# Performance work log

Measured on AMD Instinct MI355X. Metric: run time of the kernel, lower is better.

The kernel has to match this reference:

```python
import jax, jax.numpy as jnp
import numpy as np

N_NODES = 50000
N_EDGES = 800000
D_IN, D_HID, D_OUT = 64, 128, 64


def _sage_conv(x, src, dst, W_l, b_l, W_r):
    # PyG SAGEConv (aggr='mean'): out = lin_l(mean_j x_j) + lin_r(x_i)
    msg = x[src]                                    # [E, d] gather
    summed = jax.ops.segment_sum(msg, dst, num_segments=N_NODES)
    cnt = jax.ops.segment_sum(jnp.ones((msg.shape[0], 1), x.dtype), dst,
                              num_segments=N_NODES)
    mean = summed / jnp.maximum(cnt, 1.0)           # [N, d]
    return mean @ W_l + b_l + x @ W_r


def setup_inputs() -> dict:
    key = jax.random.key(0)
    ks = jax.random.split(key, 8)
    x = jax.random.normal(ks[0], (N_NODES, D_IN), dtype=jnp.float32)
    edge_index = jax.random.randint(ks[1], (2, N_EDGES), 0, N_NODES, dtype=jnp.int64)
    s1 = 1.0 / np.sqrt(D_IN)
    s2 = 1.0 / np.sqrt(D_HID)
    W_l1 = jax.random.uniform(ks[2], (D_IN, D_HID), jnp.float32, -s1, s1)
    b_l1 = jnp.zeros((D_HID,), jnp.float32)
    W_r1 = jax.random.uniform(ks[3], (D_IN, D_HID), jnp.float32, -s1, s1)
    W_l2 = jax.random.uniform(ks[4], (D_HID, D_OUT), jnp.float32, -s2, s2)
    b_l2 = jnp.zeros((D_OUT,), jnp.float32)
    W_r2 = jax.random.uniform(ks[5], (D_HID, D_OUT), jnp.float32, -s2, s2)
    return {"x": x, "edge_index": edge_index,
            "W_l1": W_l1, "b_l1": b_l1, "W_r1": W_r1,
            "W_l2": W_l2, "b_l2": b_l2, "W_r2": W_r2}


def reference(x, edge_index, W_l1, b_l1, W_r1, W_l2, b_l2, W_r2):
    src, dst = edge_index[0], edge_index[1]
    h = _sage_conv(x, src, dst, W_l1, b_l1, W_r1)
    h = jax.nn.relu(h)
    # dropout is identity in eval mode (F.dropout(training=self.training))
    out = _sage_conv(h, src, dst, W_l2, b_l2, W_r2)
    return out
```

## Files before the change

### kernel.cpp

```cpp
#include <hip/hip_runtime.h>

namespace {

constexpr int NNODES = 50000;
constexpr int NEDGES = 800000;
constexpr int NBUCK  = (NNODES + 127) / 128;
constexpr int BCAP   = 3072;
constexpr int SB     = 64;
constexpr int CHUNK  = NEDGES / SB;


static __device__ __forceinline__ unsigned short f2bf(float f) {
  unsigned u = __float_as_uint(f);
  u += 0x7FFFu + ((u >> 16) & 1u);
  return (unsigned short)(u >> 16);
}

static __device__ __forceinline__ void pk_fma_lo(float2& d, const float2 a, const float2 b) {
  asm("v_pk_fma_f32 %0, %1, %2, %0 op_sel:[0,0,0] op_sel_hi:[0,1,1]"
      : "+v"(d) : "v"(a), "v"(b));
}
static __device__ __forceinline__ void pk_fma_hi(float2& d, const float2 a, const float2 b) {
  asm("v_pk_fma_f32 %0, %1, %2, %0 op_sel:[1,0,0] op_sel_hi:[1,1,1]"
      : "+v"(d) : "v"(a), "v"(b));
}

static __device__ __forceinline__ void grid_sync(int* bar, int target) {
  __syncthreads();
  if (threadIdx.x == 0) {
    __threadfence();
    atomicAdd(bar, 1);
    while (atomicAdd(bar, 0) < target) {
      __builtin_amdgcn_s_sleep(2);
    }
    __threadfence();
  }
  __syncthreads();
}

static __device__ __forceinline__ int detect_is64_block(const void* raw, int* s_tmp) {
  if (threadIdx.x == 0) *s_tmp = 0;
  __syncthreads();
  const unsigned int* w = (const unsigned int*)raw;
  const int nz = (w[1 + 2 * (int)(threadIdx.x & 511)] != 0u) ? 1 : 0;
  if (nz) atomicOr(s_tmp, 1);
  __syncthreads();
  return (*s_tmp == 0) ? 1 : 0;
}

__global__ __launch_bounds__(512) void prep_mega(const void* __restrict__ raw,
                                                 const float* __restrict__ xin,
                                                 unsigned short* __restrict__ xb,
                                                 int* __restrict__ blkhist,
                                                 int* __restrict__ offs,
                                                 int* __restrict__ bcount,
                                                 unsigned int* __restrict__ ecol,
                                                 int* __restrict__ rowse,
                                                 int* __restrict__ bar) {
  __shared__ int hist[NBUCK];
  __shared__ int loff[NBUCK];
  __shared__ int lcur[NBUCK];
  __shared__ int dcnt[128];
  __shared__ int noff[128];
  __shared__ int ncur[128];
  __shared__ int s_tmp;

  const int b = blockIdx.x;
  const int tid = (int)threadIdx.x;
  const int is64 = detect_is64_block(raw, &s_tmp);

  for (int t = b * 512 + tid; t < NNODES * 64 / 4; t += SB * 512) {
    const float4 v = ((const float4*)xin)[t];
    ushort4 o;
    o.x = f2bf(v.x); o.y = f2bf(v.y); o.z = f2bf(v.z); o.w = f2bf(v.w);
    ((ushort4*)xb)[t] = o;
  }
  for (int i = tid; i < NBUCK; i += 512) hist[i] = 0;
  __syncthreads();
  {
    const int beg = b * CHUNK, end = beg + CHUNK;
    for (int e = beg + tid; e < end; e += 512) {
      const int d = is64 ? (int)((const long long*)raw)[NEDGES + e]
                         : ((const int*)raw)[NEDGES + e];
      atomicAdd(&hist[d >> 7], 1);
    }
  }
  __syncthreads();
  for (int i = tid; i < NBUCK; i += 512) blkhist[i * SB + b] = hist[i];

  grid_sync(bar, SB * 1);

  {
    const int lane = tid & 63;
    const int bk = b * 8 + (tid >> 6);
    if (bk < NBUCK) {
      const int c = blkhist[bk * SB + lane];
      int s = c;
#pragma unroll
      for (int off = 1; off < 64; off <<= 1) {
        const int u = __shfl_up(s, off, 64);
        if (lane >= off) s += u;
      }
      offs[bk * SB + lane] = bk * BCAP + (s - c);
      if (lane == 63) bcount[bk] = s;
    }
  }

  grid_sync(bar, SB * 2);

  for (int i = tid; i < NBUCK; i += 512) {
    loff[i] = offs[i * SB + b];
    lcur[i] = 0;
  }
  __syncthreads();
  {
    const int beg = b * CHUNK, end = beg + CHUNK;
    for (int e = beg + tid; e < end; e += 512) {
      int s, d;
      if (is64) {
        const long long* p = (const long long*)raw;
        s = (int)p[e];
        d = (int)p[NEDGES + e];
      } else {
        const int* p = (const int*)raw;
        s = p[e];
        d = p[NEDGES + e];
      }
      const int bk = d >> 7;
      const unsigned int val = ((unsigned int)d << 16) | (unsigned int)s;
      const int lr = atomicAdd(&lcur[bk], 1);
      ecol[loff[bk] + lr] = val;
    }
  }

  grid_sync(bar, SB * 3);

  for (int bk = b; bk < NBUCK; bk += SB) {
    const int base = bk * 128;
    const int nloc = min(128, NNODES - base);
    const int cnt = bcount[bk];
    unsigned int* eb = ecol + (size_t)bk * BCAP;
    if (tid < 128) dcnt[tid] = 0;
    __syncthreads();
    unsigned int vals[6];
    int m = 0;
#pragma unroll
    for (int k = 0; k < 6; ++k) {
      const int e = tid + k * 512;
      if (e < cnt) {
        vals[k] = eb[e];
        atomicAdd(&dcnt[(vals[k] >> 16) & 127u], 1);
        m = k + 1;
      }
    }
    __syncthreads();
    if (tid < 128) noff[tid] = dcnt[tid];
    __syncthreads();
#pragma unroll
    for (int off = 1; off < 128; off <<= 1) {
      int add = 0;
      if (tid < 128 && tid >= off) add = noff[tid - off];
      __syncthreads();
      if (tid < 128) noff[tid] += add;
      __syncthreads();
    }
    if (tid < 128) {
      const int excl = noff[tid] - dcnt[tid];
      noff[tid] = excl;
      ncur[tid] = 0;
      if (tid < nloc)
        rowse[base + tid] = ((bk * BCAP + excl) << 9) | dcnt[tid];
    }
    __syncthreads();
#pragma unroll
    for (int k = 0; k < 6; ++k) {
      if (k < m) {
        const int loc = (int)((vals[k] >> 16) & 127u);
        eb[noff[loc] + atomicAdd(&ncur[loc], 1)] = vals[k] & 0xFFFFu;
      }
    }
    __syncthreads();
  }
}

template <bool FINAL>
__global__ __launch_bounds__(256) void seg_mean_bf(const unsigned int* __restrict__ xb2,
                                                   const int* __restrict__ rowse,
                                                   const unsigned int* __restrict__ col,
                                                   const float* __restrict__ radd,
                                                   float* __restrict__ outbuf) {
  const int lane = (int)(threadIdx.x & 63);
  const int half = lane >> 5;
  const int c = lane & 31;
  const int wid = (blockIdx.x * blockDim.x + threadIdx.x) >> 6;
  const int nw = (gridDim.x * blockDim.x) >> 6;
  for (int v = wid; v < NNODES; v += nw) {
    const int se = rowse[v];
    const int b = se >> 9;
    const int e = b + (se & 511);
    float accx = 0.0f, accy = 0.0f;
    int i = b;
    for (; i + 8 <= e; i += 8) {
      const int s0 = (int)col[i + 0 + half];
      const int s1 = (int)col[i + 2 + half];
      const int s2 = (int)col[i + 4 + half];
      const int s3 = (int)col[i + 6 + half];
      const unsigned int w0 = xb2[(size_t)s0 * 32 + c];
      const unsigned int w1 = xb2[(size_t)s1 * 32 + c];
      const unsigned int w2 = xb2[(size_t)s2 * 32 + c];
      const unsigned int w3 = xb2[(size_t)s3 * 32 + c];
      accx += __uint_as_float(w0 << 16) + __uint_as_float(w1 << 16)
            + __uint_as_float(w2 << 16) + __uint_as_float(w3 << 16);
      accy += __uint_as_float(w0 & 0xFFFF0000u) + __uint_as_float(w1 & 0xFFFF0000u)
            + __uint_as_float(w2 & 0xFFFF0000u) + __uint_as_float(w3 & 0xFFFF0000u);
    }
    for (; i + 2 <= e; i += 2) {
      const unsigned int w0 = xb2[(size_t)col[i + half] * 32 + c];
      accx += __uint_as_float(w0 << 16);
      accy += __uint_as_float(w0 & 0xFFFF0000u);
    }
    if (i < e && half == 0) {
      const unsigned int w0 = xb2[(size_t)col[i] * 32 + c];
      accx += __uint_as_float(w0 << 16);
      accy += __uint_as_float(w0 & 0xFFFF0000u);
    }
    accx += __shfl_xor(accx, 32, 64);
    accy += __shfl_xor(accy, 32, 64);
    if (half == 0) {
      const float inv = 1.0f / fmaxf((float)(se & 511), 1.0f);
      float2 res = make_float2(accx * inv, accy * inv);
      const size_t gi = (size_t)v * 32 + c;
      if (FINAL) {
        const float2 ra = ((const float2*)radd)[gi];
        res.x += ra.x; res.y += ra.y;
      }
      ((float2*)outbuf)[gi] = res;
    }
  }
}

template <int MODE>
__global__ __launch_bounds__(256, 3) void gemm128(const float* __restrict__ A0,
                                                  const float* __restrict__ A1,
                                                  const float* __restrict__ W0,
                                                  const float* __restrict__ W1,
                                                  const float* __restrict__ bias,
                                                  float* __restrict__ O0,
                                                  float* __restrict__ O1,
                                                  unsigned short* __restrict__ PB) {
  constexpr int SAS = 36;
  __shared__ float sA[64][SAS];
  __shared__ float sW[32][128];
  const int row0 = blockIdx.x * 64;
  const int tid = threadIdx.x;
  const int r0 = (tid >> 4) * 4;
  const int j0 = (tid & 15) * 4;

  float2 accA2[4][2];
  float2 accB2[4][2];
#pragma unroll
  for (int r = 0; r < 4; ++r)
#pragma unroll
    for (int p = 0; p < 2; ++p) {
      accA2[r][p] = make_float2(0.f, 0.f);
      accB2[r][p] = make_float2(0.f, 0.f);
    }

#pragma unroll 1
  for (int ck = 0; ck < 4; ++ck) {
#pragma unroll
    for (int v = 0; v < 2; ++v) {
      const int vid = v * 256 + tid;
      const int rr = vid >> 3;
      const int kq = (vid & 7) * 4;
      const int grow = row0 + rr;
      float4 val = make_float4(0.f, 0.f, 0.f, 0.f);
      if (grow < NNODES) {
        if (MODE == 0) {
          const float* src = (ck < 2) ? A0 : A1;
          const int kk = (ck & 1) * 32 + kq;
          val = *(const float4*)&src[(size_t)grow * 64 + kk];
        } else {
          val = *(const float4*)&A0[(size_t)grow * 128 + ck * 32 + kq];
        }
      }
      *(float4*)&sA[rr][kq] = val;
    }
#pragma unroll
    for (int v = 0; v < 4; ++v) {
      const int vid = v * 256 + tid;
      const int kk = vid >> 5;
      const int jq = (vid & 31) * 4;
      float4 w;
      if (MODE == 0) {
        const float* src = (ck < 2) ? W0 : W1;
        const int krel = (ck & 1) * 32 + kk;
        w = *(const float4*)&src[(size_t)krel * 128 + jq];
      } else {
        const int kg = ck * 32 + kk;
        const float* src = (jq < 64) ? W0 : W1;
        const int jrel = (jq < 64) ? jq : jq - 64;
        w = *(const float4*)&src[(size_t)kg * 64 + jrel];
      }
      *(float4*)&sW[kk][jq] = w;
    }
    __syncthreads();
#pragma unroll
    for (int k4 = 0; k4 < 8; ++k4) {
      float4 a[4];
#pragma unroll
      for (int r = 0; r < 4; ++r) a[r] = *(const float4*)&sA[r0 + r][k4 * 4];
#pragma unroll
      for (int kp = 0; kp < 2; ++kp) {
        const int k_even = k4 * 4 + kp * 2;
        const float4 wlo0 = *(const float4*)&sW[k_even][j0];
        const float4 whi0 = *(const float4*)&sW[k_even][64 + j0];
        const float4 wlo1 = *(const float4*)&sW[k_even + 1][j0];
        const float4 whi1 = *(const float4*)&sW[k_even + 1][64 + j0];
#pragma unroll
        for (int r = 0; r < 4; ++r) {
          const float2 ap = (kp == 0) ? make_float2(a[r].x, a[r].y)
                                      : make_float2(a[r].z, a[r].w);
          pk_fma_lo(accA2[r][0], ap, make_float2(wlo0.x, wlo0.y));
          pk_fma_lo(accA2[r][1], ap, make_float2(wlo0.z, wlo0.w));
          pk_fma_lo(accB2[r][0], ap, make_float2(whi0.x, whi0.y));
          pk_fma_lo(accB2[r][1], ap, make_float2(whi0.z, whi0.w));
          pk_fma_hi(accA2[r][0], ap, make_float2(wlo1.x, wlo1.y));
          pk_fma_hi(accA2[r][1], ap, make_float2(wlo1.z, wlo1.w));
          pk_fma_hi(accB2[r][0], ap, make_float2(whi1.x, whi1.y));
          pk_fma_hi(accB2[r][1], ap, make_float2(whi1.z, whi1.w));
        }
      }
    }
    __syncthreads();
  }

  float4 blo = make_float4(0.f, 0.f, 0.f, 0.f);
  float4 bhi;
  if (MODE == 0) {
    blo = *(const float4*)&bias[j0];
    bhi = *(const float4*)&bias[64 + j0];
  } else {
    bhi = *(const float4*)&bias[j0];
  }
#pragma unroll
  for (int r = 0; r < 4; ++r) {
    const int grow = row0 + r0 + r;
    if (grow >= NNODES) continue;
    float4 lo = make_float4(accA2[r][0].x + blo.x, accA2[r][0].y + blo.y,
                            accA2[r][1].x + blo.z, accA2[r][1].y + blo.w);
    float4 hi = make_float4(accB2[r][0].x + bhi.x, accB2[r][0].y + bhi.y,
                            accB2[r][1].x + bhi.z, accB2[r][1].y + bhi.w);
    if (MODE == 0) {
      lo.x = fmaxf(lo.x, 0.f); lo.y = fmaxf(lo.y, 0.f);
      lo.z = fmaxf(lo.z, 0.f); lo.w = fmaxf(lo.w, 0.f);
      hi.x = fmaxf(hi.x, 0.f); hi.y = fmaxf(hi.y, 0.f);
      hi.z = fmaxf(hi.z, 0.f); hi.w = fmaxf(hi.w, 0.f);
      *(float4*)&O0[(size_t)grow * 128 + j0] = lo;
      *(float4*)&O0[(size_t)grow * 128 + 64 + j0] = hi;
    } else {
      ushort4 ob;
      ob.x = f2bf(lo.x); ob.y = f2bf(lo.y); ob.z = f2bf(lo.z); ob.w = f2bf(lo.w);
      *(ushort4*)&PB[(size_t)grow * 64 + j0] = ob;
      *(float4*)&O1[(size_t)grow * 64 + j0] = hi;
    }
  }
}

}

extern "C" void kernel_launch(void* const* d_in, const int* in_sizes, int n_in,
                              void* d_out, int out_size, void* d_ws, size_t ws_size,
                              hipStream_t stream) {
  const float* x   = (const float*)d_in[0];
  const void*  ei  = d_in[1];
  const float* Wl1 = (const float*)d_in[2];
  const float* bl1 = (const float*)d_in[3];
  const float* Wr1 = (const float*)d_in[4];
  const float* Wl2 = (const float*)d_in[5];
  const float* bl2 = (const float*)d_in[6];
  const float* Wr2 = (const float*)d_in[7];
  float* out = (float*)d_out;

  char* ws = (char*)d_ws;
  int*            bar     = (int*)(ws + 0);
  int*            blkhist = (int*)(ws + 256);
  int*            offs    = (int*)(ws + 100608);
  int*            bcount  = (int*)(ws + 200960);
  int*            rowse   = (int*)(ws + 203008);
  unsigned int*   ecol    = (unsigned int*)(ws + 403200);
  unsigned short* xb      = (unsigned short*)(ws + 5207808);
  unsigned short* pb      = (unsigned short*)(ws + 11607808);
  float*          mean1   = (float*)(ws + 18007808);
  float*          h       = (float*)(ws + 30807808);
  float*          r       = mean1;

  hipMemsetAsync(bar, 0, 256, stream);

  prep_mega<<<SB, 512, 0, stream>>>(ei, x, xb, blkhist, offs, bcount, ecol, rowse, bar);

  constexpr int GEMM_BLOCKS = (NNODES + 63) / 64;

  seg_mean_bf<false><<<12500, 256, 0, stream>>>((const unsigned int*)xb, rowse, ecol,
                                                nullptr, mean1);
  gemm128<0><<<GEMM_BLOCKS, 256, 0, stream>>>(mean1, x, Wl1, Wr1, bl1, h, nullptr, nullptr);

  gemm128<1><<<GEMM_BLOCKS, 256, 0, stream>>>(h, nullptr, Wl2, Wr2, bl2, nullptr, r, pb);
  seg_mean_bf<true><<<12500, 256, 0, stream>>>((const unsigned int*)pb, rowse, ecol,
                                               r, out);
}
```

Baseline: 192.2 us.

## Split prep into separate kernels and fuse both layer GEMMs through shared memory

```diff
diff --git a/kernel.cpp b/kernel.cpp
--- a/kernel.cpp
+++ b/kernel.cpp
@@ -8,6 +8,7 @@
 constexpr int BCAP   = 3072;
 constexpr int SB     = 64;
 constexpr int CHUNK  = NEDGES / SB;
+constexpr int CONVB  = 1024;
 
 
 static __device__ __forceinline__ unsigned short f2bf(float f) {
@@ -25,19 +26,6 @@
       : "+v"(d) : "v"(a), "v"(b));
 }
 
-static __device__ __forceinline__ void grid_sync(int* bar, int target) {
-  __syncthreads();
-  if (threadIdx.x == 0) {
-    __threadfence();
-    atomicAdd(bar, 1);
-    while (atomicAdd(bar, 0) < target) {
-      __builtin_amdgcn_s_sleep(2);
-    }
-    __threadfence();
-  }
-  __syncthreads();
-}
-
 static __device__ __forceinline__ int detect_is64_block(const void* raw, int* s_tmp) {
   if (threadIdx.x == 0) *s_tmp = 0;
   __syncthreads();
@@ -48,138 +36,133 @@
   return (*s_tmp == 0) ? 1 : 0;
 }
 
-__global__ __launch_bounds__(512) void prep_mega(const void* __restrict__ raw,
-                                                 const float* __restrict__ xin,
-                                                 unsigned short* __restrict__ xb,
-                                                 int* __restrict__ blkhist,
-                                                 int* __restrict__ offs,
-                                                 int* __restrict__ bcount,
-                                                 unsigned int* __restrict__ ecol,
-                                                 int* __restrict__ rowse,
-                                                 int* __restrict__ bar) {
+__global__ __launch_bounds__(512) void histconv(const void* __restrict__ raw,
+                                                const float* __restrict__ xin,
+                                                unsigned short* __restrict__ xb,
+                                                int* __restrict__ blkhist) {
+  const int tid = (int)threadIdx.x;
+  if (blockIdx.x >= SB) {
+    const int b = blockIdx.x - SB;
+    for (int t = b * 512 + tid; t < NNODES * 64 / 4; t += CONVB * 512) {
+      const float4 v = ((const float4*)xin)[t];
+      ushort4 o;
+      o.x = f2bf(v.x); o.y = f2bf(v.y); o.z = f2bf(v.z); o.w = f2bf(v.w);
+      ((ushort4*)xb)[t] = o;
+    }
+    return;
+  }
   __shared__ int hist[NBUCK];
+  __shared__ int s_tmp;
+  const int is64 = detect_is64_block(raw, &s_tmp);
+  for (int i = tid; i < NBUCK; i += 512) hist[i] = 0;
+  __syncthreads();
+  const int b = blockIdx.x;
+  const int beg = b * CHUNK, end = beg + CHUNK;
+  for (int e = beg + tid; e < end; e += 512) {
+    const int d = is64 ? (int)((const long long*)raw)[NEDGES + e]
+                       : ((const int*)raw)[NEDGES + e];
+    atomicAdd(&hist[d >> 7], 1);
+  }
+  __syncthreads();
+  for (int i = tid; i < NBUCK; i += 512) blkhist[i * SB + b] = hist[i];
+}
+
+__global__ __launch_bounds__(512) void scatter_pass(const void* __restrict__ raw,
+                                                    const int* __restrict__ blkhist,
+                                                    unsigned int* __restrict__ ecol) {
   __shared__ int loff[NBUCK];
   __shared__ int lcur[NBUCK];
+  __shared__ int s_tmp;
+  const int is64 = detect_is64_block(raw, &s_tmp);
+  const int b = blockIdx.x;
+  const int tid = (int)threadIdx.x;
+  for (int bk = tid; bk < NBUCK; bk += 512) {
+    int s = 0;
+    for (int bb = 0; bb < b; ++bb) s += blkhist[bk * SB + bb];
+    loff[bk] = bk * BCAP + s;
+    lcur[bk] = 0;
+  }
+  __syncthreads();
+  const int beg = b * CHUNK, end = beg + CHUNK;
+  for (int e = beg + tid; e < end; e += 512) {
+    int s, d;
+    if (is64) {
+      const long long* p = (const long long*)raw;
+      s = (int)p[e];
+      d = (int)p[NEDGES + e];
+    } else {
+      const int* p = (const int*)raw;
+      s = p[e];
+      d = p[NEDGES + e];
+    }
+    const int bk = d >> 7;
+    const unsigned int val = ((unsigned int)d << 16) | (unsigned int)s;
+    const int lr = atomicAdd(&lcur[bk], 1);
+    ecol[loff[bk] + lr] = val;
+  }
+}
+
+__global__ __launch_bounds__(256) void csr_emit(const int* __restrict__ blkhist,
+                                                unsigned int* __restrict__ ecol,
+                                                int* __restrict__ rowse) {
+  const int bk = blockIdx.x;
+  const int base = bk * 128;
+  const int nloc = min(128, NNODES - base);
+  const int tid = (int)threadIdx.x;
+  unsigned int* eb = ecol + (size_t)bk * BCAP;
+
   __shared__ int dcnt[128];
   __shared__ int noff[128];
   __shared__ int ncur[128];
-  __shared__ int s_tmp;
-
-  const int b = blockIdx.x;
-  const int tid = (int)threadIdx.x;
-  const int is64 = detect_is64_block(raw, &s_tmp);
-
-  for (int t = b * 512 + tid; t < NNODES * 64 / 4; t += SB * 512) {
-    const float4 v = ((const float4*)xin)[t];
-    ushort4 o;
-    o.x = f2bf(v.x); o.y = f2bf(v.y); o.z = f2bf(v.z); o.w = f2bf(v.w);
-    ((ushort4*)xb)[t] = o;
-  }
-  for (int i = tid; i < NBUCK; i += 512) hist[i] = 0;
-  __syncthreads();
-  {
-    const int beg = b * CHUNK, end = beg + CHUNK;
-    for (int e = beg + tid; e < end; e += 512) {
-      const int d = is64 ? (int)((const long long*)raw)[NEDGES + e]
-                         : ((const int*)raw)[NEDGES + e];
-      atomicAdd(&hist[d >> 7], 1);
-    }
-  }
-  __syncthreads();
-  for (int i = tid; i < NBUCK; i += 512) blkhist[i * SB + b] = hist[i];
-
-  grid_sync(bar, SB * 1);
-
-  {
-    const int lane = tid & 63;
-    const int bk = b * 8 + (tid >> 6);
-    if (bk < NBUCK) {
-      const int c = blkhist[bk * SB + lane];
-      int s = c;
-#pragma unroll
-      for (int off = 1; off < 64; off <<= 1) {
-        const int u = __shfl_up(s, off, 64);
-        if (lane >= off) s += u;
-      }
-      offs[bk * SB + lane] = bk * BCAP + (s - c);
-      if (lane == 63) bcount[bk] = s;
-    }
-  }
-
-  grid_sync(bar, SB * 2);
-
-  for (int i = tid; i < NBUCK; i += 512) {
-    loff[i] = offs[i * SB + b];
-    lcur[i] = 0;
-  }
-  __syncthreads();
-  {
-    const int beg = b * CHUNK, end = beg + CHUNK;
-    for (int e = beg + tid; e < end; e += 512) {
-      int s, d;
-      if (is64) {
-        const long long* p = (const long long*)raw;
-        s = (int)p[e];
-        d = (int)p[NEDGES + e];
-      } else {
-        const int* p = (const int*)raw;
-        s = p[e];
-        d = p[NEDGES + e];
-      }
-      const int bk = d >> 7;
-      const unsigned int val = ((unsigned int)d << 16) | (unsigned int)s;
-      const int lr = atomicAdd(&lcur[bk], 1);
-      ecol[loff[bk] + lr] = val;
-    }
-  }
-
-  grid_sync(bar, SB * 3);
-
-  for (int bk = b; bk < NBUCK; bk += SB) {
-    const int base = bk * 128;
-    const int nloc = min(128, NNODES - base);
-    const int cnt = bcount[bk];
-    unsigned int* eb = ecol + (size_t)bk * BCAP;
-    if (tid < 128) dcnt[tid] = 0;
-    __syncthreads();
-    unsigned int vals[6];
-    int m = 0;
-#pragma unroll
-    for (int k = 0; k < 6; ++k) {
-      const int e = tid + k * 512;
-      if (e < cnt) {
-        vals[k] = eb[e];
-        atomicAdd(&dcnt[(vals[k] >> 16) & 127u], 1);
-        m = k + 1;
-      }
-    }
-    __syncthreads();
-    if (tid < 128) noff[tid] = dcnt[tid];
-    __syncthreads();
-#pragma unroll
-    for (int off = 1; off < 128; off <<= 1) {
-      int add = 0;
-      if (tid < 128 && tid >= off) add = noff[tid - off];
-      __syncthreads();
-      if (tid < 128) noff[tid] += add;
-      __syncthreads();
-    }
-    if (tid < 128) {
-      const int excl = noff[tid] - dcnt[tid];
-      noff[tid] = excl;
-      ncur[tid] = 0;
-      if (tid < nloc)
-        rowse[base + tid] = ((bk * BCAP + excl) << 9) | dcnt[tid];
-    }
-    __syncthreads();
-#pragma unroll
-    for (int k = 0; k < 6; ++k) {
-      if (k < m) {
-        const int loc = (int)((vals[k] >> 16) & 127u);
-        eb[noff[loc] + atomicAdd(&ncur[loc], 1)] = vals[k] & 0xFFFFu;
-      }
-    }
-    __syncthreads();
+  __shared__ int s_cnt;
+  if (tid < 64) {
+    int c = blkhist[bk * SB + tid];
+#pragma unroll
+    for (int off = 32; off; off >>= 1) c += __shfl_down(c, off, 64);
+    if (tid == 0) s_cnt = c;
+  }
+  if (tid < 128) dcnt[tid] = 0;
+  __syncthreads();
+  const int cnt = s_cnt;
+
+  unsigned int vals[12];
+  int m = 0;
+#pragma unroll
+  for (int k = 0; k < 12; ++k) {
+    const int e = tid + k * 256;
+    if (e < cnt) {
+      vals[k] = eb[e];
+      atomicAdd(&dcnt[(vals[k] >> 16) & 127u], 1);
+      m = k + 1;
+    }
+  }
+  __syncthreads();
+
+  if (tid < 128) noff[tid] = dcnt[tid];
+  __syncthreads();
+#pragma unroll
+  for (int off = 1; off < 128; off <<= 1) {
+    int add = 0;
+    if (tid < 128 && tid >= off) add = noff[tid - off];
+    __syncthreads();
+    if (tid < 128) noff[tid] += add;
+    __syncthreads();
+  }
+  if (tid < 128) {
+    const int excl = noff[tid] - dcnt[tid];
+    noff[tid] = excl;
+    ncur[tid] = 0;
+    if (tid < nloc)
+      rowse[base + tid] = ((bk * BCAP + excl) << 9) | dcnt[tid];
+  }
+  __syncthreads();
+
+#pragma unroll
+  for (int k = 0; k < 12; ++k) {
+    if (k < m) {
+      const int loc = (int)((vals[k] >> 16) & 127u);
+      eb[noff[loc] + atomicAdd(&ncur[loc], 1)] = vals[k] & 0xFFFFu;
+    }
   }
 }
 
@@ -239,18 +222,21 @@
   }
 }
 
-template <int MODE>
-__global__ __launch_bounds__(256, 3) void gemm128(const float* __restrict__ A0,
-                                                  const float* __restrict__ A1,
-                                                  const float* __restrict__ W0,
-                                                  const float* __restrict__ W1,
-                                                  const float* __restrict__ bias,
-                                                  float* __restrict__ O0,
-                                                  float* __restrict__ O1,
-                                                  unsigned short* __restrict__ PB) {
+__global__ __launch_bounds__(256, 2) void gemm_fused(const float* __restrict__ MEAN1,
+                                                     const float* __restrict__ X,
+                                                     const float* __restrict__ Wl1,
+                                                     const float* __restrict__ Wr1,
+                                                     const float* __restrict__ bl1,
+                                                     const float* __restrict__ Wl2,
+                                                     const float* __restrict__ Wr2,
+                                                     const float* __restrict__ bl2,
+                                                     unsigned short* __restrict__ PB,
+                                                     float* __restrict__ R) {
   constexpr int SAS = 36;
+  constexpr int SHS = 132;
   __shared__ float sA[64][SAS];
   __shared__ float sW[32][128];
+  __shared__ float sH[64][SHS];
   const int row0 = blockIdx.x * 64;
   const int tid = threadIdx.x;
   const int r0 = (tid >> 4) * 4;
@@ -276,13 +262,9 @@
       const int grow = row0 + rr;
       float4 val = make_float4(0.f, 0.f, 0.f, 0.f);
       if (grow < NNODES) {
-        if (MODE == 0) {
-          const float* src = (ck < 2) ? A0 : A1;
-          const int kk = (ck & 1) * 32 + kq;
-          val = *(const float4*)&src[(size_t)grow * 64 + kk];
-        } else {
-          val = *(const float4*)&A0[(size_t)grow * 128 + ck * 32 + kq];
-        }
+        const float* src = (ck < 2) ? MEAN1 : X;
+        const int kk = (ck & 1) * 32 + kq;
+        val = *(const float4*)&src[(size_t)grow * 64 + kk];
       }
       *(float4*)&sA[rr][kq] = val;
     }
@@ -291,18 +273,9 @@
       const int vid = v * 256 + tid;
       const int kk = vid >> 5;
       const int jq = (vid & 31) * 4;
-      float4 w;
-      if (MODE == 0) {
-        const float* src = (ck < 2) ? W0 : W1;
-        const int krel = (ck & 1) * 32 + kk;
-        w = *(const float4*)&src[(size_t)krel * 128 + jq];
-      } else {
-        const int kg = ck * 32 + kk;
-        const float* src = (jq < 64) ? W0 : W1;
-        const int jrel = (jq < 64) ? jq : jq - 64;
-        w = *(const float4*)&src[(size_t)kg * 64 + jrel];
-      }
-      *(float4*)&sW[kk][jq] = w;
+      const float* src = (ck < 2) ? Wl1 : Wr1;
+      const int krel = (ck & 1) * 32 + kk;
+      *(float4*)&sW[kk][jq] = *(const float4*)&src[(size_t)krel * 128 + jq];
     }
     __syncthreads();
 #pragma unroll
@@ -335,34 +308,83 @@
     __syncthreads();
   }
 
-  float4 blo = make_float4(0.f, 0.f, 0.f, 0.f);
-  float4 bhi;
-  if (MODE == 0) {
-    blo = *(const float4*)&bias[j0];
-    bhi = *(const float4*)&bias[64 + j0];
-  } else {
-    bhi = *(const float4*)&bias[j0];
-  }
-#pragma unroll
-  for (int r = 0; r < 4; ++r) {
-    const int grow = row0 + r0 + r;
-    if (grow >= NNODES) continue;
-    float4 lo = make_float4(accA2[r][0].x + blo.x, accA2[r][0].y + blo.y,
-                            accA2[r][1].x + blo.z, accA2[r][1].y + blo.w);
-    float4 hi = make_float4(accB2[r][0].x + bhi.x, accB2[r][0].y + bhi.y,
-                            accB2[r][1].x + bhi.z, accB2[r][1].y + bhi.w);
-    if (MODE == 0) {
-      lo.x = fmaxf(lo.x, 0.f); lo.y = fmaxf(lo.y, 0.f);
-      lo.z = fmaxf(lo.z, 0.f); lo.w = fmaxf(lo.w, 0.f);
-      hi.x = fmaxf(hi.x, 0.f); hi.y = fmaxf(hi.y, 0.f);
-      hi.z = fmaxf(hi.z, 0.f); hi.w = fmaxf(hi.w, 0.f);
-      *(float4*)&O0[(size_t)grow * 128 + j0] = lo;
-      *(float4*)&O0[(size_t)grow * 128 + 64 + j0] = hi;
-    } else {
+  {
+    const float4 blo = *(const float4*)&bl1[j0];
+    const float4 bhi = *(const float4*)&bl1[64 + j0];
+#pragma unroll
+    for (int r = 0; r < 4; ++r) {
+      float4 lo = make_float4(fmaxf(accA2[r][0].x + blo.x, 0.f),
+                              fmaxf(accA2[r][0].y + blo.y, 0.f),
+                              fmaxf(accA2[r][1].x + blo.z, 0.f),
+                              fmaxf(accA2[r][1].y + blo.w, 0.f));
+      float4 hi = make_float4(fmaxf(accB2[r][0].x + bhi.x, 0.f),
+                              fmaxf(accB2[r][0].y + bhi.y, 0.f),
+                              fmaxf(accB2[r][1].x + bhi.z, 0.f),
+                              fmaxf(accB2[r][1].y + bhi.w, 0.f));
+      *(float4*)&sH[r0 + r][j0] = lo;
+      *(float4*)&sH[r0 + r][64 + j0] = hi;
+      accA2[r][0] = make_float2(0.f, 0.f); accA2[r][1] = make_float2(0.f, 0.f);
+      accB2[r][0] = make_float2(0.f, 0.f); accB2[r][1] = make_float2(0.f, 0.f);
+    }
+  }
+  __syncthreads();
+
+#pragma unroll 1
+  for (int ck = 0; ck < 4; ++ck) {
+#pragma unroll
+    for (int v = 0; v < 4; ++v) {
+      const int vid = v * 256 + tid;
+      const int kk = vid >> 5;
+      const int jq = (vid & 31) * 4;
+      const int kg = ck * 32 + kk;
+      const float* src = (jq < 64) ? Wl2 : Wr2;
+      const int jrel = (jq < 64) ? jq : jq - 64;
+      *(float4*)&sW[kk][jq] = *(const float4*)&src[(size_t)kg * 64 + jrel];
+    }
+    __syncthreads();
+#pragma unroll
+    for (int k4 = 0; k4 < 8; ++k4) {
+      float4 a[4];
+#pragma unroll
+      for (int r = 0; r < 4; ++r) a[r] = *(const float4*)&sH[r0 + r][ck * 32 + k4 * 4];
+#pragma unroll
+      for (int kp = 0; kp < 2; ++kp) {
+        const int k_even = k4 * 4 + kp * 2;
+        const float4 wlo0 = *(const float4*)&sW[k_even][j0];
+        const float4 whi0 = *(const float4*)&sW[k_even][64 + j0];
+        const float4 wlo1 = *(const float4*)&sW[k_even + 1][j0];
+        const float4 whi1 = *(const float4*)&sW[k_even + 1][64 + j0];
+#pragma unroll
+        for (int r = 0; r < 4; ++r) {
+          const float2 ap = (kp == 0) ? make_float2(a[r].x, a[r].y)
+                                      : make_float2(a[r].z, a[r].w);
+          pk_fma_lo(accA2[r][0], ap, make_float2(wlo0.x, wlo0.y));
+          pk_fma_lo(accA2[r][1], ap, make_float2(wlo0.z, wlo0.w));
+          pk_fma_lo(accB2[r][0], ap, make_float2(whi0.x, whi0.y));
+          pk_fma_lo(accB2[r][1], ap, make_float2(whi0.z, whi0.w));
+          pk_fma_hi(accA2[r][0], ap, make_float2(wlo1.x, wlo1.y));
+          pk_fma_hi(accA2[r][1], ap, make_float2(wlo1.z, wlo1.w));
+          pk_fma_hi(accB2[r][0], ap, make_float2(whi1.x, whi1.y));
+          pk_fma_hi(accB2[r][1], ap, make_float2(whi1.z, whi1.w));
+        }
+      }
+    }
+    __syncthreads();
+  }
+
+  {
+    const float4 bhi = *(const float4*)&bl2[j0];
+#pragma unroll
+    for (int r = 0; r < 4; ++r) {
+      const int grow = row0 + r0 + r;
+      if (grow >= NNODES) continue;
       ushort4 ob;
-      ob.x = f2bf(lo.x); ob.y = f2bf(lo.y); ob.z = f2bf(lo.z); ob.w = f2bf(lo.w);
+      ob.x = f2bf(accA2[r][0].x); ob.y = f2bf(accA2[r][0].y);
+      ob.z = f2bf(accA2[r][1].x); ob.w = f2bf(accA2[r][1].y);
       *(ushort4*)&PB[(size_t)grow * 64 + j0] = ob;
-      *(float4*)&O1[(size_t)grow * 64 + j0] = hi;
+      float4 hi = make_float4(accB2[r][0].x + bhi.x, accB2[r][0].y + bhi.y,
+                              accB2[r][1].x + bhi.z, accB2[r][1].y + bhi.w);
+      *(float4*)&R[(size_t)grow * 64 + j0] = hi;
     }
   }
 }
@@ -383,29 +405,24 @@
   float* out = (float*)d_out;
 
   char* ws = (char*)d_ws;
-  int*            bar     = (int*)(ws + 0);
-  int*            blkhist = (int*)(ws + 256);
-  int*            offs    = (int*)(ws + 100608);
-  int*            bcount  = (int*)(ws + 200960);
-  int*            rowse   = (int*)(ws + 203008);
-  unsigned int*   ecol    = (unsigned int*)(ws + 403200);
-  unsigned short* xb      = (unsigned short*)(ws + 5207808);
-  unsigned short* pb      = (unsigned short*)(ws + 11607808);
-  float*          mean1   = (float*)(ws + 18007808);
-  float*          h       = (float*)(ws + 30807808);
+  int*            blkhist = (int*)(ws + 0);
+  int*            rowse   = (int*)(ws + 100352);
+  unsigned int*   ecol    = (unsigned int*)(ws + 301056);
+  unsigned short* xb      = (unsigned short*)(ws + 5105664);
+  unsigned short* pb      = (unsigned short*)(ws + 11505664);
+  float*          mean1   = (float*)(ws + 17905664);
   float*          r       = mean1;
 
-  hipMemsetAsync(bar, 0, 256, stream);
-
-  prep_mega<<<SB, 512, 0, stream>>>(ei, x, xb, blkhist, offs, bcount, ecol, rowse, bar);
+  histconv<<<SB + CONVB, 512, 0, stream>>>(ei, x, xb, blkhist);
+  scatter_pass<<<SB, 512, 0, stream>>>(ei, blkhist, ecol);
+  csr_emit<<<NBUCK, 256, 0, stream>>>(blkhist, ecol, rowse);
 
   constexpr int GEMM_BLOCKS = (NNODES + 63) / 64;
 
   seg_mean_bf<false><<<12500, 256, 0, stream>>>((const unsigned int*)xb, rowse, ecol,
                                                 nullptr, mean1);
-  gemm128<0><<<GEMM_BLOCKS, 256, 0, stream>>>(mean1, x, Wl1, Wr1, bl1, h, nullptr, nullptr);
-
-  gemm128<1><<<GEMM_BLOCKS, 256, 0, stream>>>(h, nullptr, Wl2, Wr2, bl2, nullptr, r, pb);
+  gemm_fused<<<GEMM_BLOCKS, 256, 0, stream>>>(mean1, x, Wl1, Wr1, bl1,
+                                              Wl2, Wr2, bl2, pb, r);
   seg_mean_bf<true><<<12500, 256, 0, stream>>>((const unsigned int*)pb, rowse, ecol,
                                                r, out);
 }
```

New measurement: 167.6 us. 1.15x faster.

## Split persistent prep kernel into separate launches, removing grid barriers

Applied to the files above, without the earlier changes.

```diff
diff --git a/kernel.cpp b/kernel.cpp
--- a/kernel.cpp
+++ b/kernel.cpp
@@ -8,6 +8,7 @@
 constexpr int BCAP   = 3072;
 constexpr int SB     = 64;
 constexpr int CHUNK  = NEDGES / SB;
+constexpr int CONVB  = 1024;
 
 
 static __device__ __forceinline__ unsigned short f2bf(float f) {
@@ -25,19 +26,6 @@
       : "+v"(d) : "v"(a), "v"(b));
 }
 
-static __device__ __forceinline__ void grid_sync(int* bar, int target) {
-  __syncthreads();
-  if (threadIdx.x == 0) {
-    __threadfence();
-    atomicAdd(bar, 1);
-    while (atomicAdd(bar, 0) < target) {
-      __builtin_amdgcn_s_sleep(2);
-    }
-    __threadfence();
-  }
-  __syncthreads();
-}
-
 static __device__ __forceinline__ int detect_is64_block(const void* raw, int* s_tmp) {
   if (threadIdx.x == 0) *s_tmp = 0;
   __syncthreads();
@@ -48,138 +36,133 @@
   return (*s_tmp == 0) ? 1 : 0;
 }
 
-__global__ __launch_bounds__(512) void prep_mega(const void* __restrict__ raw,
-                                                 const float* __restrict__ xin,
-                                                 unsigned short* __restrict__ xb,
-                                                 int* __restrict__ blkhist,
-                                                 int* __restrict__ offs,
-                                                 int* __restrict__ bcount,
-                                                 unsigned int* __restrict__ ecol,
-                                                 int* __restrict__ rowse,
-                                                 int* __restrict__ bar) {
+__global__ __launch_bounds__(512) void histconv(const void* __restrict__ raw,
+                                                const float* __restrict__ xin,
+                                                unsigned short* __restrict__ xb,
+                                                int* __restrict__ blkhist) {
+  const int tid = (int)threadIdx.x;
+  if (blockIdx.x >= SB) {
+    const int b = blockIdx.x - SB;
+    for (int t = b * 512 + tid; t < NNODES * 64 / 4; t += CONVB * 512) {
+      const float4 v = ((const float4*)xin)[t];
+      ushort4 o;
+      o.x = f2bf(v.x); o.y = f2bf(v.y); o.z = f2bf(v.z); o.w = f2bf(v.w);
+      ((ushort4*)xb)[t] = o;
+    }
+    return;
+  }
   __shared__ int hist[NBUCK];
+  __shared__ int s_tmp;
+  const int is64 = detect_is64_block(raw, &s_tmp);
+  for (int i = tid; i < NBUCK; i += 512) hist[i] = 0;
+  __syncthreads();
+  const int b = blockIdx.x;
+  const int beg = b * CHUNK, end = beg + CHUNK;
+  for (int e = beg + tid; e < end; e += 512) {
+    const int d = is64 ? (int)((const long long*)raw)[NEDGES + e]
+                       : ((const int*)raw)[NEDGES + e];
+    atomicAdd(&hist[d >> 7], 1);
+  }
+  __syncthreads();
+  for (int i = tid; i < NBUCK; i += 512) blkhist[i * SB + b] = hist[i];
+}
+
+__global__ __launch_bounds__(512) void scatter_pass(const void* __restrict__ raw,
+                                                    const int* __restrict__ blkhist,
+                                                    unsigned int* __restrict__ ecol) {
   __shared__ int loff[NBUCK];
   __shared__ int lcur[NBUCK];
+  __shared__ int s_tmp;
+  const int is64 = detect_is64_block(raw, &s_tmp);
+  const int b = blockIdx.x;
+  const int tid = (int)threadIdx.x;
+  for (int bk = tid; bk < NBUCK; bk += 512) {
+    int s = 0;
+    for (int bb = 0; bb < b; ++bb) s += blkhist[bk * SB + bb];
+    loff[bk] = bk * BCAP + s;
+    lcur[bk] = 0;
+  }
+  __syncthreads();
+  const int beg = b * CHUNK, end = beg + CHUNK;
+  for (int e = beg + tid; e < end; e += 512) {
+    int s, d;
+    if (is64) {
+      const long long* p = (const long long*)raw;
+      s = (int)p[e];
+      d = (int)p[NEDGES + e];
+    } else {
+      const int* p = (const int*)raw;
+      s = p[e];
+      d = p[NEDGES + e];
+    }
+    const int bk = d >> 7;
+    const unsigned int val = ((unsigned int)d << 16) | (unsigned int)s;
+    const int lr = atomicAdd(&lcur[bk], 1);
+    ecol[loff[bk] + lr] = val;
+  }
+}
+
+__global__ __launch_bounds__(256) void csr_emit(const int* __restrict__ blkhist,
+                                                unsigned int* __restrict__ ecol,
+                                                int* __restrict__ rowse) {
+  const int bk = blockIdx.x;
+  const int base = bk * 128;
+  const int nloc = min(128, NNODES - base);
+  const int tid = (int)threadIdx.x;
+  unsigned int* eb = ecol + (size_t)bk * BCAP;
+
   __shared__ int dcnt[128];
   __shared__ int noff[128];
   __shared__ int ncur[128];
-  __shared__ int s_tmp;
-
-  const int b = blockIdx.x;
-  const int tid = (int)threadIdx.x;
-  const int is64 = detect_is64_block(raw, &s_tmp);
-
-  for (int t = b * 512 + tid; t < NNODES * 64 / 4; t += SB * 512) {
-    const float4 v = ((const float4*)xin)[t];
-    ushort4 o;
-    o.x = f2bf(v.x); o.y = f2bf(v.y); o.z = f2bf(v.z); o.w = f2bf(v.w);
-    ((ushort4*)xb)[t] = o;
-  }
-  for (int i = tid; i < NBUCK; i += 512) hist[i] = 0;
-  __syncthreads();
-  {
-    const int beg = b * CHUNK, end = beg + CHUNK;
-    for (int e = beg + tid; e < end; e += 512) {
-      const int d = is64 ? (int)((const long long*)raw)[NEDGES + e]
-                         : ((const int*)raw)[NEDGES + e];
-      atomicAdd(&hist[d >> 7], 1);
-    }
-  }
-  __syncthreads();
-  for (int i = tid; i < NBUCK; i += 512) blkhist[i * SB + b] = hist[i];
-
-  grid_sync(bar, SB * 1);
-
-  {
-    const int lane = tid & 63;
-    const int bk = b * 8 + (tid >> 6);
-    if (bk < NBUCK) {
-      const int c = blkhist[bk * SB + lane];
-      int s = c;
-#pragma unroll
-      for (int off = 1; off < 64; off <<= 1) {
-        const int u = __shfl_up(s, off, 64);
-        if (lane >= off) s += u;
-      }
-      offs[bk * SB + lane] = bk * BCAP + (s - c);
-      if (lane == 63) bcount[bk] = s;
-    }
-  }
-
-  grid_sync(bar, SB * 2);
-
-  for (int i = tid; i < NBUCK; i += 512) {
-    loff[i] = offs[i * SB + b];
-    lcur[i] = 0;
-  }
-  __syncthreads();
-  {
-    const int beg = b * CHUNK, end = beg + CHUNK;
-    for (int e = beg + tid; e < end; e += 512) {
-      int s, d;
-      if (is64) {
-        const long long* p = (const long long*)raw;
-        s = (int)p[e];
-        d = (int)p[NEDGES + e];
-      } else {
-        const int* p = (const int*)raw;
-        s = p[e];
-        d = p[NEDGES + e];
-      }
-      const int bk = d >> 7;
-      const unsigned int val = ((unsigned int)d << 16) | (unsigned int)s;
-      const int lr = atomicAdd(&lcur[bk], 1);
-      ecol[loff[bk] + lr] = val;
-    }
-  }
-
-  grid_sync(bar, SB * 3);
-
-  for (int bk = b; bk < NBUCK; bk += SB) {
-    const int base = bk * 128;
-    const int nloc = min(128, NNODES - base);
-    const int cnt = bcount[bk];
-    unsigned int* eb = ecol + (size_t)bk * BCAP;
-    if (tid < 128) dcnt[tid] = 0;
+  __shared__ int s_cnt;
+  if (tid < 64) {
+    int c = blkhist[bk * SB + tid];
+#pragma unroll
+    for (int off = 32; off; off >>= 1) c += __shfl_down(c, off, 64);
+    if (tid == 0) s_cnt = c;
+  }
+  if (tid < 128) dcnt[tid] = 0;
+  __syncthreads();
+  const int cnt = s_cnt;
+
+  unsigned int vals[12];
+  int m = 0;
+#pragma unroll
+  for (int k = 0; k < 12; ++k) {
+    const int e = tid + k * 256;
+    if (e < cnt) {
+      vals[k] = eb[e];
+      atomicAdd(&dcnt[(vals[k] >> 16) & 127u], 1);
+      m = k + 1;
+    }
+  }
+  __syncthreads();
+
+  if (tid < 128) noff[tid] = dcnt[tid];
+  __syncthreads();
+#pragma unroll
+  for (int off = 1; off < 128; off <<= 1) {
+    int add = 0;
+    if (tid < 128 && tid >= off) add = noff[tid - off];
     __syncthreads();
-    unsigned int vals[6];
-    int m = 0;
-#pragma unroll
-    for (int k = 0; k < 6; ++k) {
-      const int e = tid + k * 512;
-      if (e < cnt) {
-        vals[k] = eb[e];
-        atomicAdd(&dcnt[(vals[k] >> 16) & 127u], 1);
-        m = k + 1;
-      }
-    }
+    if (tid < 128) noff[tid] += add;
     __syncthreads();
-    if (tid < 128) noff[tid] = dcnt[tid];
-    __syncthreads();
-#pragma unroll
-    for (int off = 1; off < 128; off <<= 1) {
-      int add = 0;
-      if (tid < 128 && tid >= off) add = noff[tid - off];
-      __syncthreads();
-      if (tid < 128) noff[tid] += add;
-      __syncthreads();
-    }
-    if (tid < 128) {
-      const int excl = noff[tid] - dcnt[tid];
-      noff[tid] = excl;
-      ncur[tid] = 0;
-      if (tid < nloc)
-        rowse[base + tid] = ((bk * BCAP + excl) << 9) | dcnt[tid];
-    }
-    __syncthreads();
-#pragma unroll
-    for (int k = 0; k < 6; ++k) {
-      if (k < m) {
-        const int loc = (int)((vals[k] >> 16) & 127u);
-        eb[noff[loc] + atomicAdd(&ncur[loc], 1)] = vals[k] & 0xFFFFu;
-      }
-    }
-    __syncthreads();
+  }
+  if (tid < 128) {
+    const int excl = noff[tid] - dcnt[tid];
+    noff[tid] = excl;
+    ncur[tid] = 0;
+    if (tid < nloc)
+      rowse[base + tid] = ((bk * BCAP + excl) << 9) | dcnt[tid];
+  }
+  __syncthreads();
+
+#pragma unroll
+  for (int k = 0; k < 12; ++k) {
+    if (k < m) {
+      const int loc = (int)((vals[k] >> 16) & 127u);
+      eb[noff[loc] + atomicAdd(&ncur[loc], 1)] = vals[k] & 0xFFFFu;
+    }
   }
 }
 
@@ -383,28 +366,24 @@
   float* out = (float*)d_out;
 
   char* ws = (char*)d_ws;
-  int*            bar     = (int*)(ws + 0);
-  int*            blkhist = (int*)(ws + 256);
-  int*            offs    = (int*)(ws + 100608);
-  int*            bcount  = (int*)(ws + 200960);
-  int*            rowse   = (int*)(ws + 203008);
-  unsigned int*   ecol    = (unsigned int*)(ws + 403200);
-  unsigned short* xb      = (unsigned short*)(ws + 5207808);
-  unsigned short* pb      = (unsigned short*)(ws + 11607808);
-  float*          mean1   = (float*)(ws + 18007808);
-  float*          h       = (float*)(ws + 30807808);
+  int*            blkhist = (int*)(ws + 0);
+  int*            rowse   = (int*)(ws + 100352);
+  unsigned int*   ecol    = (unsigned int*)(ws + 301056);
+  unsigned short* xb      = (unsigned short*)(ws + 5105664);
+  unsigned short* pb      = (unsigned short*)(ws + 11505664);
+  float*          mean1   = (float*)(ws + 17905664);
+  float*          h       = (float*)(ws + 30705664);
   float*          r       = mean1;
 
-  hipMemsetAsync(bar, 0, 256, stream);
-
-  prep_mega<<<SB, 512, 0, stream>>>(ei, x, xb, blkhist, offs, bcount, ecol, rowse, bar);
+  histconv<<<SB + CONVB, 512, 0, stream>>>(ei, x, xb, blkhist);
+  scatter_pass<<<SB, 512, 0, stream>>>(ei, blkhist, ecol);
+  csr_emit<<<NBUCK, 256, 0, stream>>>(blkhist, ecol, rowse);
 
   constexpr int GEMM_BLOCKS = (NNODES + 63) / 64;
 
   seg_mean_bf<false><<<12500, 256, 0, stream>>>((const unsigned int*)xb, rowse, ecol,
                                                 nullptr, mean1);
   gemm128<0><<<GEMM_BLOCKS, 256, 0, stream>>>(mean1, x, Wl1, Wr1, bl1, h, nullptr, nullptr);
-
   gemm128<1><<<GEMM_BLOCKS, 256, 0, stream>>>(h, nullptr, Wl2, Wr2, bl2, nullptr, r, pb);
   seg_mean_bf<true><<<12500, 256, 0, stream>>>((const unsigned int*)pb, rowse, ecol,
                                                r, out);
```

Result: faster. 159.1 us (-17.2%).
